# Performance work log

Measured on AMD Instinct MI355X. Metric: run time of the kernel, lower is better.

The kernel has to match this reference:

```python
import jax, jax.numpy as jnp
import numpy as np

N, IN_DIM, OUT_DIM = 256, 1024, 1024
DROP_P = 0.5

def setup_inputs() -> dict:
    key = jax.random.key(0)
    k1, k2, k3, k4, k5 = jax.random.split(key, 5)
    x = jax.random.normal(k1, (N, IN_DIM), dtype=jnp.float32)
    weight = jax.random.normal(k2, (IN_DIM, OUT_DIM), dtype=jnp.float32) / np.sqrt(IN_DIM)
    bias = jax.random.normal(k3, (OUT_DIM,), dtype=jnp.float32)
    # binary keep-masks, as in torch.rand(...).gt(p).to(dtype)
    w_mask = (jax.random.uniform(k4, (N, IN_DIM, OUT_DIM)) > DROP_P).astype(jnp.float32)
    b_mask = (jax.random.uniform(k5, (N, OUT_DIM)) > DROP_P).astype(jnp.float32)
    return {"x": x, "weight": weight, "bias": bias, "w_mask": w_mask, "b_mask": b_mask}

def reference(x, weight, bias, w_mask, b_mask):
    # training path of DropConnect: per-sample masked weight matmul
    # y[n,o] = sum_k x[n,k] * weight[k,o] * w_mask[n,k,o]  + bias[o]*b_mask[n,o], scaled by 1/(1-p)
    y = jnp.einsum('nk,ko,nko->no', x, weight, w_mask) + bias[None, :] * b_mask
    return y * (1.0 / (1.0 - DROP_P))
```

## Files before the change

### kernel.cpp

```cpp
#include <hip/hip_runtime.h>


constexpr int N_      = 256;
constexpr int IN_DIM  = 1024;
constexpr int OUT_DIM = 1024;

typedef float f32x4 __attribute__((ext_vector_type(4)));

__global__ __launch_bounds__(256, 4) void dropconnect_kernel(
    const float* __restrict__ x,
    const float* __restrict__ weight,
    const float* __restrict__ bias,
    const float* __restrict__ w_mask,
    const float* __restrict__ b_mask,
    float* __restrict__ out)
{
    const int n = blockIdx.x;
    const int t = threadIdx.x;

    const size_t row4 = (size_t)n * IN_DIM * (OUT_DIM / 4);
    const f32x4* __restrict__ wm = reinterpret_cast<const f32x4*>(w_mask) + row4 + t;
    const f32x4* __restrict__ wt = reinterpret_cast<const f32x4*>(weight) + t;
    const float* __restrict__ xr = x + n * IN_DIM;

    f32x4 acc = {0.f, 0.f, 0.f, 0.f};

    #pragma unroll 8
    for (int k = 0; k < IN_DIM; ++k) {
        const float xv = xr[k];
        const f32x4 m = __builtin_nontemporal_load(wm + (size_t)k * (OUT_DIM / 4));
        const f32x4 w = wt[k * (OUT_DIM / 4)];
        acc[0] = fmaf(xv * w[0], m[0], acc[0]);
        acc[1] = fmaf(xv * w[1], m[1], acc[1]);
        acc[2] = fmaf(xv * w[2], m[2], acc[2]);
        acc[3] = fmaf(xv * w[3], m[3], acc[3]);
    }

    const f32x4 bm = reinterpret_cast<const f32x4*>(b_mask)[n * (OUT_DIM / 4) + t];
    const f32x4 bs = reinterpret_cast<const f32x4*>(bias)[t];
    f32x4 r;
    r[0] = 2.0f * (acc[0] + bs[0] * bm[0]);
    r[1] = 2.0f * (acc[1] + bs[1] * bm[1]);
    r[2] = 2.0f * (acc[2] + bs[2] * bm[2]);
    r[3] = 2.0f * (acc[3] + bs[3] * bm[3]);
    reinterpret_cast<f32x4*>(out)[n * (OUT_DIM / 4) + t] = r;
}

extern "C" void kernel_launch(void* const* d_in, const int* in_sizes, int n_in,
                              void* d_out, int out_size, void* d_ws, size_t ws_size,
                              hipStream_t stream) {
    const float* x      = (const float*)d_in[0];
    const float* weight = (const float*)d_in[1];
    const float* bias   = (const float*)d_in[2];
    const float* w_mask = (const float*)d_in[3];
    const float* b_mask = (const float*)d_in[4];
    float* out = (float*)d_out;

    dim3 grid(N_);
    dim3 block(256);
    dropconnect_kernel<<<grid, block, 0, stream>>>(x, weight, bias, w_mask, b_mask, out);
}
```

Baseline: 204.1 us.

## Split K reduction across four thread groups per block with LDS reduce

```diff
diff --git a/kernel.cpp b/kernel.cpp
--- a/kernel.cpp
+++ b/kernel.cpp
@@ -4,10 +4,13 @@
 constexpr int N_      = 256;
 constexpr int IN_DIM  = 1024;
 constexpr int OUT_DIM = 1024;
+constexpr int O4      = OUT_DIM / 4;
+constexpr int KSPLIT  = 4;
+constexpr int KCHUNK  = IN_DIM / KSPLIT;
 
 typedef float f32x4 __attribute__((ext_vector_type(4)));
 
-__global__ __launch_bounds__(256, 4) void dropconnect_kernel(
+__global__ __launch_bounds__(1024, 4) void dropconnect_kernel(
     const float* __restrict__ x,
     const float* __restrict__ weight,
     const float* __restrict__ bias,
@@ -15,35 +18,49 @@
     const float* __restrict__ b_mask,
     float* __restrict__ out)
 {
-    const int n = blockIdx.x;
-    const int t = threadIdx.x;
+    __shared__ f32x4 red[1024];
 
-    const size_t row4 = (size_t)n * IN_DIM * (OUT_DIM / 4);
-    const f32x4* __restrict__ wm = reinterpret_cast<const f32x4*>(w_mask) + row4 + t;
-    const f32x4* __restrict__ wt = reinterpret_cast<const f32x4*>(weight) + t;
-    const float* __restrict__ xr = x + n * IN_DIM;
+    const int n  = blockIdx.x;
+    const int t  = threadIdx.x;
+    const int ks = t >> 8;
+    const int c4 = t & 255;
+
+    const size_t base4 = ((size_t)n * IN_DIM + (size_t)ks * KCHUNK) * O4;
+    const f32x4* __restrict__ wm = reinterpret_cast<const f32x4*>(w_mask) + base4 + c4;
+    const f32x4* __restrict__ wt = reinterpret_cast<const f32x4*>(weight) + (size_t)ks * KCHUNK * O4 + c4;
+    const float* __restrict__ xr = x + n * IN_DIM + ks * KCHUNK;
 
     f32x4 acc = {0.f, 0.f, 0.f, 0.f};
 
     #pragma unroll 8
-    for (int k = 0; k < IN_DIM; ++k) {
+    for (int k = 0; k < KCHUNK; ++k) {
         const float xv = xr[k];
-        const f32x4 m = __builtin_nontemporal_load(wm + (size_t)k * (OUT_DIM / 4));
-        const f32x4 w = wt[k * (OUT_DIM / 4)];
+        const f32x4 m = __builtin_nontemporal_load(wm + (size_t)k * O4);
+        const f32x4 w = wt[k * O4];
         acc[0] = fmaf(xv * w[0], m[0], acc[0]);
         acc[1] = fmaf(xv * w[1], m[1], acc[1]);
         acc[2] = fmaf(xv * w[2], m[2], acc[2]);
         acc[3] = fmaf(xv * w[3], m[3], acc[3]);
     }
 
-    const f32x4 bm = reinterpret_cast<const f32x4*>(b_mask)[n * (OUT_DIM / 4) + t];
-    const f32x4 bs = reinterpret_cast<const f32x4*>(bias)[t];
-    f32x4 r;
-    r[0] = 2.0f * (acc[0] + bs[0] * bm[0]);
-    r[1] = 2.0f * (acc[1] + bs[1] * bm[1]);
-    r[2] = 2.0f * (acc[2] + bs[2] * bm[2]);
-    r[3] = 2.0f * (acc[3] + bs[3] * bm[3]);
-    reinterpret_cast<f32x4*>(out)[n * (OUT_DIM / 4) + t] = r;
+    red[t] = acc;
+    __syncthreads();
+
+    if (t < 256) {
+        const f32x4 a0 = red[t];
+        const f32x4 a1 = red[t + 256];
+        const f32x4 a2 = red[t + 512];
+        const f32x4 a3 = red[t + 768];
+
+        const f32x4 bm = reinterpret_cast<const f32x4*>(b_mask)[n * O4 + t];
+        const f32x4 bs = reinterpret_cast<const f32x4*>(bias)[t];
+        f32x4 r;
+        r[0] = 2.0f * ((a0[0] + a1[0]) + (a2[0] + a3[0]) + bs[0] * bm[0]);
+        r[1] = 2.0f * ((a0[1] + a1[1]) + (a2[1] + a3[1]) + bs[1] * bm[1]);
+        r[2] = 2.0f * ((a0[2] + a1[2]) + (a2[2] + a3[2]) + bs[2] * bm[2]);
+        r[3] = 2.0f * ((a0[3] + a1[3]) + (a2[3] + a3[3]) + bs[3] * bm[3]);
+        reinterpret_cast<f32x4*>(out)[n * O4 + t] = r;
+    }
 }
 
 extern "C" void kernel_launch(void* const* d_in, const int* in_sizes, int n_in,
@@ -57,6 +74,6 @@
     float* out = (float*)d_out;
 
     dim3 grid(N_);
-    dim3 block(256);
+    dim3 block(KSPLIT * 256);
     dropconnect_kernel<<<grid, block, 0, stream>>>(x, weight, bias, w_mask, b_mask, out);
 }
```

After: 187.0 us. -8.4%, faster.
